# Kernel optimization log

Measured on AMD Instinct MI355X. Metric: run time of the kernel, lower is better.

The kernel has to match this reference:

```python
import jax, jax.numpy as jnp
import numpy as np

B, T, I = 64, 512, 512
H, L = 512, 2


def setup_inputs() -> dict:
    key = jax.random.key(0)
    ks = jax.random.split(key, 5)
    s = 1.0 / np.sqrt(H)
    return {
        "x": jax.random.normal(ks[0], (B, T, I), dtype=jnp.float32),
        "h0": jnp.zeros((L, B, H), dtype=jnp.float32),
        "Wih": jax.random.uniform(ks[1], (L, H, I), dtype=jnp.float32, minval=-s, maxval=s),
        "bih": jax.random.uniform(ks[2], (L, H), dtype=jnp.float32, minval=-s, maxval=s),
        "Whh": jax.random.uniform(ks[3], (L, H, H), dtype=jnp.float32, minval=-s, maxval=s),
        "bhh": jax.random.uniform(ks[4], (L, H), dtype=jnp.float32, minval=-s, maxval=s),
    }


def reference(x, h0, Wih, bih, Whh, bhh):
    # x: [B, T, I] (batch_first) -> scan over time axis
    xt = jnp.swapaxes(x, 0, 1)  # [T, B, I]

    def step(hidden, x_t):
        # hidden: [L, B, H], x_t: [B, I]
        inp = x_t
        new_h = []
        for l in range(L):
            h = jnp.tanh(inp @ Wih[l].T + bih[l] + hidden[l] @ Whh[l].T + bhh[l])
            new_h.append(h)
            inp = h  # dropout=0.0 -> identity between layers
        return jnp.stack(new_h, axis=0), inp

    hidden_final, outs = jax.lax.scan(step, h0, xt)
    outputs = jnp.swapaxes(outs, 0, 1)  # [B, T, H]
    return outputs, hidden_final
```

## Files before the change

kernel.cpp:

```cpp
#include <hip/hip_runtime.h>
#include <hip/hip_fp16.h>

#define HD 512
#define Bsz 64
#define Tlen 512
#define GB 4
#define RING 16

typedef _Float16 h2v __attribute__((ext_vector_type(2)));
typedef unsigned u32x4 __attribute__((ext_vector_type(4)));
typedef unsigned long long ull;

__device__ __forceinline__ float dot2acc(unsigned a, unsigned b, float c) {
    return __builtin_amdgcn_fdot2(__builtin_bit_cast(h2v, a),
                                  __builtin_bit_cast(h2v, b), c, false);
}

__device__ __forceinline__ u32x4 mall_ld16(const void* p) {
    u32x4 r;
    asm volatile("global_load_dwordx4 %0, %1, off sc0 sc1\n\ts_waitcnt vmcnt(0)"
                 : "=v"(r) : "v"(p) : "memory");
    return r;
}
__device__ __forceinline__ void mall_st16(void* p, u32x4 v) {
    asm volatile("global_store_dwordx4 %0, %1, off sc0 sc1"
                 :: "v"(p), "v"(v) : "memory");
}
__device__ __forceinline__ unsigned mall_ld4(const unsigned* p) {
    unsigned r;
    asm volatile("global_load_dword %0, %1, off sc0 sc1\n\ts_waitcnt vmcnt(0)"
                 : "=v"(r) : "v"(p) : "memory");
    return r;
}
__device__ __forceinline__ void mall_st4(unsigned* p, unsigned v) {
    asm volatile("global_store_dword %0, %1, off sc0 sc1"
                 :: "v"(p), "v"(v) : "memory");
}

__device__ __forceinline__ void probe_ld16(u32x4* d, const void* p) {
    asm volatile("global_load_dwordx4 %0, %1, off sc0 sc1"
                 : "=v"(*d) : "v"(p) : "memory");
}
__device__ __forceinline__ void probe_wait(u32x4* d) {
    asm volatile("s_waitcnt vmcnt(0)" : "+v"(*d) :: "memory");
}

__device__ __forceinline__ bool valid8(u32x4 v) {
    unsigned bad = 0;
#pragma unroll
    for (int i = 0; i < 4; ++i) {
        bad |= ((v[i] & 0xFFFFu) == 0xFFFFu);
        bad |= ((v[i] >> 16)     == 0xFFFFu);
    }
    return bad == 0u;
}

__device__ __forceinline__ u32x4 probe_finish(u32x4 v, const void* p) {
    bool ok = valid8(v);
    for (;;) {
        if (!__any((int)(!ok))) break;
        __builtin_amdgcn_s_sleep(1);
        if (!ok) { v = mall_ld16(p); ok = valid8(v); }
    }
    return v;
}

__device__ __forceinline__ u32x4 ring_wait16(const void* p) {
    u32x4 v;
    bool ok = false;
    for (;;) {
        if (!ok) { v = mall_ld16(p); ok = valid8(v); }
        if (!__any((int)(!ok))) break;
        __builtin_amdgcn_s_sleep(1);
    }
    return v;
}

__device__ __forceinline__ void cvt4s(_Float16* d, float4 v) {
    union { ull u; _Float16 h[4]; } t;
    t.h[0] = (_Float16)v.x; t.h[1] = (_Float16)v.y;
    t.h[2] = (_Float16)v.z; t.h[3] = (_Float16)v.w;
    *(ull*)d = t.u;
}

__device__ __forceinline__ void gemm4(const u32x4* __restrict__ Ip, const u32x4* wr,
                                      int kq, int kbase, float acc[2][4]) {
#pragma unroll
    for (int i = 0; i < 4; ++i) {
        const int k8 = kbase + kq + 16 * i;
        const u32x4 w0 = wr[i * 2 + 0], w1 = wr[i * 2 + 1];
#pragma unroll
        for (int b = 0; b < 4; ++b) {
            const u32x4 h = Ip[b * 128 + k8];
#pragma unroll
            for (int e = 0; e < 4; ++e) {
                acc[0][b] = dot2acc(w0[e], h[e], acc[0][b]);
                acc[1][b] = dot2acc(w1[e], h[e], acc[1][b]);
            }
        }
    }
}

__global__ __launch_bounds__(512, 1) void rnn_fullring(
    const float* __restrict__ x, const float* __restrict__ h0in,
    const float* __restrict__ Wih, const float* __restrict__ bih,
    const float* __restrict__ Whh, const float* __restrict__ bhh,
    _Float16* __restrict__ H0r, _Float16* __restrict__ H1r,
    float* __restrict__ out)
{
    __shared__ _Float16 inb[GB * 128 * 8] __attribute__((aligned(16)));
    __shared__ float    part[256 * 17];
    __shared__ _Float16 hout[256] __attribute__((aligned(16)));

    const int bid = blockIdx.x;
    const int g   = bid & 15;
    const int sl  = bid >> 4;
    const int l   = sl >> 3;
    const int rb  = sl & 7;
    const int tid = threadIdx.x;
    const int rh = tid >> 8, kq = (tid >> 4) & 15, rq = tid & 15;

    u32x4 wreg[16];
    {
        const float* WI = Wih + (size_t)l * HD * HD;
        const float* WH = Whh + (size_t)l * HD * HD;
#pragma unroll
        for (int ph = 0; ph < 2; ++ph) {
            const float* W = ph ? WH : WI;
#pragma unroll
            for (int i = 0; i < 4; ++i)
#pragma unroll
                for (int ri = 0; ri < 2; ++ri) {
                    const int row = rb * 64 + rq + 16 * (2 * rh + ri);
                    const float* p = W + (size_t)row * HD + (kq + 16 * i) * 8;
                    union { u32x4 u; _Float16 h[8]; } v;
#pragma unroll
                    for (int e = 0; e < 8; ++e) v.h[e] = (_Float16)p[e];
                    wreg[ph * 8 + i * 2 + ri] = v.u;
                }
        }
    }

    float bias = 0.f;
    if (tid < 256) {
        const int rowg = rb * 64 + (tid & 63);
        bias = bih[l * HD + rowg] + bhh[l * HD + rowg];
    }

    _Float16* ringo = l ? H1r : H0r;
    const u32x4* Ip = (const u32x4*)inb;

    const int bb = tid >> 7;
    const int k4 = tid & 127;
    const int bglobS = g * GB + bb;
    const int b2 = (tid >> 6) & 3;
    const int k8 = tid & 63;

    float4 xreg;
    if (l == 0) xreg = *(const float4*)(x + (size_t)bglobS * Tlen * HD + k4 * 4);

    for (int t = 0; t < Tlen; ++t) {
        float acc[2][4] = {{0, 0, 0, 0}, {0, 0, 0, 0}};

        if (l == 0) {
            cvt4s(&inb[(bb * 128 + (k4 >> 1)) * 8 + (k4 & 1) * 4], xreg);
            __syncthreads();
            const _Float16* hp = H0r + ((size_t)(t - 1) * Bsz + g * GB + b2) * HD + k8 * 8;
            u32x4 pv;
            if (t == 0) {
                if (tid < 256) {
                    const float* src = h0in + (size_t)(g * GB + b2) * HD + k8 * 8;
                    cvt4s(&inb[(b2 * 128 + 64 + k8) * 8],     *(const float4*)src);
                    cvt4s(&inb[(b2 * 128 + 64 + k8) * 8 + 4], *(const float4*)(src + 4));
                }
            } else if (tid < 256) {
                probe_ld16(&pv, hp);
            }
            if (t + 1 < Tlen)
                xreg = *(const float4*)(x + ((size_t)bglobS * Tlen + t + 1) * HD + k4 * 4);
            gemm4(Ip, wreg, kq, 0, acc);
            if (t > 0 && tid < 256) {
                probe_wait(&pv);
                u32x4 v = probe_finish(pv, hp);
                *(u32x4*)&inb[(b2 * 128 + 64 + k8) * 8] = v;
            }
            __syncthreads();
            gemm4(Ip, wreg + 8, kq, 64, acc);
        } else {
            const _Float16* hp1 = H1r + ((size_t)(t - 1) * Bsz + g * GB + b2) * HD + k8 * 8;
            u32x4 pv;
            if (tid >= 256) {
                if (t == 0) {
                    const float* src = h0in + (size_t)(Bsz + g * GB + b2) * HD + k8 * 8;
                    cvt4s(&inb[(b2 * 128 + 64 + k8) * 8],     *(const float4*)src);
                    cvt4s(&inb[(b2 * 128 + 64 + k8) * 8 + 4], *(const float4*)(src + 4));
                } else {
                    probe_ld16(&pv, hp1);
                }
            } else {
                u32x4 v = ring_wait16(H0r + ((size_t)t * Bsz + g * GB + b2) * HD + k8 * 8);
                *(u32x4*)&inb[(b2 * 128 + k8) * 8] = v;
            }
            __syncthreads();
            gemm4(Ip, wreg, kq, 0, acc);
            if (t > 0 && tid >= 256) {
                probe_wait(&pv);
                u32x4 v = probe_finish(pv, hp1);
                *(u32x4*)&inb[(b2 * 128 + 64 + k8) * 8] = v;
            }
            __syncthreads();
            gemm4(Ip, wreg + 8, kq, 64, acc);
        }

#pragma unroll
        for (int ri = 0; ri < 2; ++ri)
#pragma unroll
            for (int b = 0; b < 4; ++b)
                part[(size_t)(b * 64 + rq + 16 * (2 * rh + ri)) * 17 + kq] = acc[ri][b];
        __syncthreads();
        if (tid < 256) {
            float s = bias;
#pragma unroll
            for (int k2 = 0; k2 < 16; ++k2) s += part[(size_t)tid * 17 + k2];
            const float hv = tanhf(s);
            hout[tid] = (_Float16)hv;
            const int rowg = rb * 64 + (tid & 63);
            const int bo = g * GB + (tid >> 6);
            if (l == 1) out[((size_t)bo * Tlen + t) * HD + rowg] = hv;
            if (t == Tlen - 1)
                out[(size_t)Bsz * Tlen * HD + ((size_t)l * Bsz + bo) * HD + rowg] = hv;
        }
        __syncthreads();

        if (tid < 32) {
            u32x4 v = *(const u32x4*)&hout[(tid >> 3) * 64 + (tid & 7) * 8];
            mall_st16(ringo + ((size_t)t * Bsz + g * GB + (tid >> 3)) * HD + rb * 64 + (tid & 7) * 8, v);
        }
    }
}

__device__ __forceinline__ void poll2(unsigned* a, unsigned* b) {
    const int ln = threadIdx.x;
    unsigned* fp = nullptr;
    if (ln < 8)       { if (a) fp = a + ln; }
    else if (ln < 16) { if (b) fp = b + (ln - 8); }
    for (;;) {
        unsigned v = fp ? mall_ld4(fp) : 1u;
        if (!__any((int)(v != 1u))) break;
        __builtin_amdgcn_s_sleep(1);
    }
}

__global__ __launch_bounds__(512, 1) void rnn_chain(
    const float* __restrict__ x, const float* __restrict__ h0in,
    const float* __restrict__ Wih, const float* __restrict__ bih,
    const float* __restrict__ Whh, const float* __restrict__ bhh,
    _Float16* __restrict__ H0r, _Float16* __restrict__ H1r,
    unsigned* f0, unsigned* f1, float* __restrict__ out)
{
    __shared__ _Float16 inb[GB * 128 * 8] __attribute__((aligned(16)));
    __shared__ float    part[256 * 17];
    __shared__ _Float16 hout[256] __attribute__((aligned(16)));

    const int bid = blockIdx.x;
    const int g   = bid & 15;
    const int sl  = bid >> 4;
    const int l   = sl >> 3;
    const int rb  = sl & 7;
    const int tid = threadIdx.x;
    const int rh = tid >> 8, kq = (tid >> 4) & 15, rq = tid & 15;

    u32x4 wreg[16];
    {
        const float* WI = Wih + (size_t)l * HD * HD;
        const float* WH = Whh + (size_t)l * HD * HD;
#pragma unroll
        for (int ph = 0; ph < 2; ++ph) {
            const float* W = ph ? WH : WI;
#pragma unroll
            for (int i = 0; i < 4; ++i)
#pragma unroll
                for (int ri = 0; ri < 2; ++ri) {
                    const int row = rb * 64 + rq + 16 * (2 * rh + ri);
                    const float* p = W + (size_t)row * HD + (kq + 16 * i) * 8;
                    union { u32x4 u; _Float16 h[8]; } v;
#pragma unroll
                    for (int e = 0; e < 8; ++e) v.h[e] = (_Float16)p[e];
                    wreg[ph * 8 + i * 2 + ri] = v.u;
                }
        }
    }

    float bias = 0.f;
    if (tid < 256) {
        const int rowg = rb * 64 + (tid & 63);
        bias = bih[l * HD + rowg] + bhh[l * HD + rowg];
    }

    unsigned* fown = (l ? f1 : f0) + ((size_t)g * Tlen) * 8 + rb;
    _Float16* ringo = l ? H1r : H0r;
    const u32x4* Ip = (const u32x4*)inb;

    const int bb = tid >> 7;
    const int k4 = tid & 127;
    const int bglobS = g * GB + bb;

    float4 xreg;
    if (l == 0) xreg = *(const float4*)(x + (size_t)bglobS * Tlen * HD + k4 * 4);

    for (int t = 0; t < Tlen; ++t) {
        const int slot = t & (RING - 1);
        float acc[2][4] = {{0, 0, 0, 0}, {0, 0, 0, 0}};

        if (l == 0) {
            cvt4s(&inb[(bb * 128 + (k4 >> 1)) * 8 + (k4 & 1) * 4], xreg);
            __syncthreads();
            if (t + 1 < Tlen)
                xreg = *(const float4*)(x + ((size_t)bglobS * Tlen + t + 1) * HD + k4 * 4);
            gemm4(Ip, wreg, kq, 0, acc);
            if (tid < 64)
                poll2((t > 0)     ? f0 + ((size_t)g * Tlen + (t - 1)) * 8 : nullptr,
                      (t >= RING) ? f1 + ((size_t)g * Tlen + (t - RING)) * 8 : nullptr);
            __syncthreads();
            if (t == 0) {
                if (tid < 256) {
                    int c2 = tid >> 6, c8 = tid & 63;
                    const float* src = h0in + (size_t)(g * GB + c2) * HD + c8 * 8;
                    cvt4s(&inb[(c2 * 128 + 64 + c8) * 8],     *(const float4*)src);
                    cvt4s(&inb[(c2 * 128 + 64 + c8) * 8 + 4], *(const float4*)(src + 4));
                }
            } else if (tid < 256) {
                int c2 = tid >> 6, c8 = tid & 63;
                u32x4 v = mall_ld16(H0r + ((size_t)((t - 1) & (RING - 1)) * Bsz + g * GB + c2) * HD + c8 * 8);
                *(u32x4*)&inb[(c2 * 128 + 64 + c8) * 8] = v;
            }
            __syncthreads();
            gemm4(Ip, wreg + 8, kq, 64, acc);
        } else {
            if (tid < 64)
                poll2(f0 + ((size_t)g * Tlen + t) * 8,
                      (t > 0) ? f1 + ((size_t)g * Tlen + (t - 1)) * 8 : nullptr);
            __syncthreads();
            if (tid < 256) {
                int c2 = tid >> 6, c8 = tid & 63;
                u32x4 v = mall_ld16(H0r + ((size_t)slot * Bsz + g * GB + c2) * HD + c8 * 8);
                *(u32x4*)&inb[(c2 * 128 + c8) * 8] = v;
            } else if (t == 0) {
                int t2 = tid - 256; int c2 = t2 >> 6, c8 = t2 & 63;
                const float* src = h0in + (size_t)(Bsz + g * GB + c2) * HD + c8 * 8;
                cvt4s(&inb[(c2 * 128 + 64 + c8) * 8],     *(const float4*)src);
                cvt4s(&inb[(c2 * 128 + 64 + c8) * 8 + 4], *(const float4*)(src + 4));
            } else {
                int t2 = tid - 256; int c2 = t2 >> 6, c8 = t2 & 63;
                u32x4 v = mall_ld16(H1r + ((size_t)((t - 1) & (RING - 1)) * Bsz + g * GB + c2) * HD + c8 * 8);
                *(u32x4*)&inb[(c2 * 128 + 64 + c8) * 8] = v;
            }
            __syncthreads();
            gemm4(Ip, wreg, kq, 0, acc);
            gemm4(Ip, wreg + 8, kq, 64, acc);
        }

#pragma unroll
        for (int ri = 0; ri < 2; ++ri)
#pragma unroll
            for (int b = 0; b < 4; ++b)
                part[(size_t)(b * 64 + rq + 16 * (2 * rh + ri)) * 17 + kq] = acc[ri][b];
        __syncthreads();
        if (tid < 256) {
            float s = bias;
#pragma unroll
            for (int k2 = 0; k2 < 16; ++k2) s += part[(size_t)tid * 17 + k2];
            const float hv = tanhf(s);
            hout[tid] = (_Float16)hv;
            const int rowg = rb * 64 + (tid & 63);
            const int bo = g * GB + (tid >> 6);
            if (l == 1) out[((size_t)bo * Tlen + t) * HD + rowg] = hv;
            if (t == Tlen - 1)
                out[(size_t)Bsz * Tlen * HD + ((size_t)l * Bsz + bo) * HD + rowg] = hv;
        }
        __syncthreads();

        if (tid < 32) {
            u32x4 v = *(const u32x4*)&hout[(tid >> 3) * 64 + (tid & 7) * 8];
            mall_st16(ringo + ((size_t)slot * Bsz + g * GB + (tid >> 3)) * HD + rb * 64 + (tid & 7) * 8, v);
        }
        if (tid < 64) {
            asm volatile("s_waitcnt vmcnt(0)" ::: "memory");
            if (tid == 0) mall_st4(fown + (size_t)t * 8, 1u);
        }
    }
}

extern "C" void kernel_launch(void* const* d_in, const int* in_sizes, int n_in,
                              void* d_out, int out_size, void* d_ws, size_t ws_size,
                              hipStream_t stream) {
    const float* x   = (const float*)d_in[0];
    const float* h0  = (const float*)d_in[1];
    const float* Wih = (const float*)d_in[2];
    const float* bih = (const float*)d_in[3];
    const float* Whh = (const float*)d_in[4];
    const float* bhh = (const float*)d_in[5];
    float* out = (float*)d_out;
    char* ws = (char*)d_ws;

    const size_t ring_bytes = (size_t)Tlen * Bsz * HD * sizeof(_Float16);

    if (ws_size >= 2 * ring_bytes) {
        _Float16* H0r = (_Float16*)ws;
        _Float16* H1r = (_Float16*)(ws + ring_bytes);
        (void)hipMemsetAsync(ws, 0xFF, 2 * ring_bytes, stream);
        void* args[] = { (void*)&x, (void*)&h0, (void*)&Wih, (void*)&bih,
                         (void*)&Whh, (void*)&bhh, (void*)&H0r, (void*)&H1r,
                         (void*)&out };
        (void)hipLaunchCooperativeKernel((const void*)rnn_fullring, dim3(256),
                                         dim3(512), args, 0, stream);
    } else {
        unsigned* f0  = (unsigned*)ws;
        unsigned* f1  = (unsigned*)(ws + (256u << 10));
        _Float16* H0r = (_Float16*)(ws + (512u << 10));
        _Float16* H1r = (_Float16*)(ws + (512u << 10) + (1u << 20));
        (void)hipMemsetAsync(ws, 0, 512u << 10, stream);
        void* args[] = { (void*)&x, (void*)&h0, (void*)&Wih, (void*)&bih,
                         (void*)&Whh, (void*)&bhh, (void*)&H0r, (void*)&H1r,
                         (void*)&f0, (void*)&f1, (void*)&out };
        (void)hipLaunchCooperativeKernel((const void*)rnn_chain, dim3(256),
                                         dim3(512), args, 0, stream);
    }
}
```

Before: 1.451 ms.

## Precompute next step's input projection off the recurrent critical path

Moves the input-half GEMM (x or layer-0 hidden times Wih) for step t+1 to the end of step t, after the hidden state is published. Each step's critical path then only waits for the recurrent h(t-1) and runs the Whh half. The overlapped probe loads are replaced by a plain ring_wait. Layer 1 now waits for layer-0 output one step early, which could add stalls if layer 0 lags behind.

```diff
diff --git a/kernel.cpp b/kernel.cpp
--- a/kernel.cpp
+++ b/kernel.cpp
@@ -37,14 +37,6 @@
                  :: "v"(p), "v"(v) : "memory");
 }
 
-__device__ __forceinline__ void probe_ld16(u32x4* d, const void* p) {
-    asm volatile("global_load_dwordx4 %0, %1, off sc0 sc1"
-                 : "=v"(*d) : "v"(p) : "memory");
-}
-__device__ __forceinline__ void probe_wait(u32x4* d) {
-    asm volatile("s_waitcnt vmcnt(0)" : "+v"(*d) :: "memory");
-}
-
 __device__ __forceinline__ bool valid8(u32x4 v) {
     unsigned bad = 0;
 #pragma unroll
@@ -53,16 +45,6 @@
         bad |= ((v[i] >> 16)     == 0xFFFFu);
     }
     return bad == 0u;
-}
-
-__device__ __forceinline__ u32x4 probe_finish(u32x4 v, const void* p) {
-    bool ok = valid8(v);
-    for (;;) {
-        if (!__any((int)(!ok))) break;
-        __builtin_amdgcn_s_sleep(1);
-        if (!ok) { v = mall_ld16(p); ok = valid8(v); }
-    }
-    return v;
 }
 
 __device__ __forceinline__ u32x4 ring_wait16(const void* p) {
@@ -156,61 +138,46 @@
     const int b2 = (tid >> 6) & 3;
     const int k8 = tid & 63;
 
+    float ih[2][4];
     float4 xreg;
-    if (l == 0) xreg = *(const float4*)(x + (size_t)bglobS * Tlen * HD + k4 * 4);
+
+    if (l == 0) {
+        xreg = *(const float4*)(x + (size_t)bglobS * Tlen * HD + k4 * 4);
+        cvt4s(&inb[(bb * 128 + (k4 >> 1)) * 8 + (k4 & 1) * 4], xreg);
+        __syncthreads();
+        xreg = *(const float4*)(x + ((size_t)bglobS * Tlen + 1) * HD + k4 * 4);
+    } else {
+        if (tid < 256) {
+            u32x4 v = ring_wait16(H0r + ((size_t)(g * GB + b2)) * HD + k8 * 8);
+            *(u32x4*)&inb[(b2 * 128 + k8) * 8] = v;
+        }
+        __syncthreads();
+    }
+#pragma unroll
+    for (int ri = 0; ri < 2; ++ri)
+#pragma unroll
+        for (int b = 0; b < 4; ++b) ih[ri][b] = 0.f;
+    gemm4(Ip, wreg, kq, 0, ih);
 
     for (int t = 0; t < Tlen; ++t) {
-        float acc[2][4] = {{0, 0, 0, 0}, {0, 0, 0, 0}};
-
-        if (l == 0) {
-            cvt4s(&inb[(bb * 128 + (k4 >> 1)) * 8 + (k4 & 1) * 4], xreg);
-            __syncthreads();
-            const _Float16* hp = H0r + ((size_t)(t - 1) * Bsz + g * GB + b2) * HD + k8 * 8;
-            u32x4 pv;
+        if (tid < 256) {
             if (t == 0) {
-                if (tid < 256) {
-                    const float* src = h0in + (size_t)(g * GB + b2) * HD + k8 * 8;
-                    cvt4s(&inb[(b2 * 128 + 64 + k8) * 8],     *(const float4*)src);
-                    cvt4s(&inb[(b2 * 128 + 64 + k8) * 8 + 4], *(const float4*)(src + 4));
-                }
-            } else if (tid < 256) {
-                probe_ld16(&pv, hp);
-            }
-            if (t + 1 < Tlen)
-                xreg = *(const float4*)(x + ((size_t)bglobS * Tlen + t + 1) * HD + k4 * 4);
-            gemm4(Ip, wreg, kq, 0, acc);
-            if (t > 0 && tid < 256) {
-                probe_wait(&pv);
-                u32x4 v = probe_finish(pv, hp);
+                const float* src = h0in + (size_t)(l * Bsz + g * GB + b2) * HD + k8 * 8;
+                cvt4s(&inb[(b2 * 128 + 64 + k8) * 8],     *(const float4*)src);
+                cvt4s(&inb[(b2 * 128 + 64 + k8) * 8 + 4], *(const float4*)(src + 4));
+            } else {
+                u32x4 v = ring_wait16(ringo + ((size_t)(t - 1) * Bsz + g * GB + b2) * HD + k8 * 8);
                 *(u32x4*)&inb[(b2 * 128 + 64 + k8) * 8] = v;
             }
-            __syncthreads();
-            gemm4(Ip, wreg + 8, kq, 64, acc);
-        } else {
-            const _Float16* hp1 = H1r + ((size_t)(t - 1) * Bsz + g * GB + b2) * HD + k8 * 8;
-            u32x4 pv;
-            if (tid >= 256) {
-                if (t == 0) {
-                    const float* src = h0in + (size_t)(Bsz + g * GB + b2) * HD + k8 * 8;
-                    cvt4s(&inb[(b2 * 128 + 64 + k8) * 8],     *(const float4*)src);
-                    cvt4s(&inb[(b2 * 128 + 64 + k8) * 8 + 4], *(const float4*)(src + 4));
-                } else {
-                    probe_ld16(&pv, hp1);
-                }
-            } else {
-                u32x4 v = ring_wait16(H0r + ((size_t)t * Bsz + g * GB + b2) * HD + k8 * 8);
-                *(u32x4*)&inb[(b2 * 128 + k8) * 8] = v;
-            }
-            __syncthreads();
-            gemm4(Ip, wreg, kq, 0, acc);
-            if (t > 0 && tid >= 256) {
-                probe_wait(&pv);
-                u32x4 v = probe_finish(pv, hp1);
-                *(u32x4*)&inb[(b2 * 128 + 64 + k8) * 8] = v;
-            }
-            __syncthreads();
-            gemm4(Ip, wreg + 8, kq, 64, acc);
-        }
+        }
+        __syncthreads();
+
+        float acc[2][4];
+#pragma unroll
+        for (int ri = 0; ri < 2; ++ri)
+#pragma unroll
+            for (int b = 0; b < 4; ++b) acc[ri][b] = ih[ri][b];
+        gemm4(Ip, wreg + 8, kq, 64, acc);
 
 #pragma unroll
         for (int ri = 0; ri < 2; ++ri)
@@ -235,6 +202,23 @@
         if (tid < 32) {
             u32x4 v = *(const u32x4*)&hout[(tid >> 3) * 64 + (tid & 7) * 8];
             mall_st16(ringo + ((size_t)t * Bsz + g * GB + (tid >> 3)) * HD + rb * 64 + (tid & 7) * 8, v);
+        }
+
+        if (t + 1 < Tlen) {
+            if (l == 0) {
+                cvt4s(&inb[(bb * 128 + (k4 >> 1)) * 8 + (k4 & 1) * 4], xreg);
+                if (t + 2 < Tlen)
+                    xreg = *(const float4*)(x + ((size_t)bglobS * Tlen + t + 2) * HD + k4 * 4);
+            } else if (tid < 256) {
+                u32x4 v = ring_wait16(H0r + ((size_t)(t + 1) * Bsz + g * GB + b2) * HD + k8 * 8);
+                *(u32x4*)&inb[(b2 * 128 + k8) * 8] = v;
+            }
+            __syncthreads();
+#pragma unroll
+            for (int ri = 0; ri < 2; ++ri)
+#pragma unroll
+                for (int b = 0; b < 4; ++b) ih[ri][b] = 0.f;
+            gemm4(Ip, wreg, kq, 0, ih);
         }
     }
 }
```

Result: faster. 1.258 ms (-13.3%).
